# Performance work log

Hardware: AMD Instinct MI355X
Metric: run time of the kernel (lower is better)

Reference implementation:

```python
import jax, jax.numpy as jnp
import numpy as np

N_NODES = 50000
N_EDGES = 400000
D_IN, D_HID, D_LAT = 1024, 512, 256


def setup_inputs() -> dict:
    key = jax.random.key(0)
    k = jax.random.split(key, 6)
    x = jax.random.normal(k[0], (N_NODES, D_IN), dtype=jnp.float32)
    edge_index = jax.random.randint(k[1], (2, N_EDGES), 0, N_NODES, dtype=jnp.int32)
    # normalized adjacency weights (e.g., D^-1/2 A D^-1/2 values), positive
    edge_weight = jax.random.uniform(k[2], (N_EDGES,), dtype=jnp.float32)
    # Glorot-style init as in GCNConv.reset_parameters
    W1 = jax.random.normal(k[3], (D_IN, D_HID), dtype=jnp.float32) * (1.0 / np.sqrt(D_IN))
    b1 = jnp.zeros((D_HID,), dtype=jnp.float32)
    W2 = jax.random.normal(k[4], (D_HID, D_LAT), dtype=jnp.float32) * (1.0 / np.sqrt(D_HID))
    b2 = jnp.zeros((D_LAT,), dtype=jnp.float32)
    return {"x": x, "edge_index": edge_index, "edge_weight": edge_weight,
            "W1": W1, "b1": b1, "W2": W2, "b2": b2}


def _gcn_layer(h, src, dst, w, W, b):
    # GCNConv: spmm(adj, h @ W) + b
    s = h @ W                                   # [N, D_out] dense GEMM
    msg = s[src] * w[:, None]                   # [E, D_out] gather + scale
    agg = jax.ops.segment_sum(msg, dst, num_segments=N_NODES)  # scatter-add
    return agg + b


def reference(x, edge_index, edge_weight, W1, b1, W2, b2):
    # eval mode: F.dropout(training=False) is identity
    src, dst = edge_index[0], edge_index[1]
    h = jax.nn.relu(_gcn_layer(x, src, dst, edge_weight, W1, b1))
    out = jax.nn.relu(_gcn_layer(h, src, dst, edge_weight, W2, b2))
    return out
```

## Files before the change

kernel.cpp:

```cpp
#include <hip/hip_runtime.h>

typedef __attribute__((ext_vector_type(8))) short short8;
typedef __attribute__((ext_vector_type(4))) float floatx4;

#define GLOBAL_AS __attribute__((address_space(1)))
#define LDS_AS __attribute__((address_space(3)))

__device__ __forceinline__ void gload_lds16(const void* g, void* l) {
  __builtin_amdgcn_global_load_lds((const GLOBAL_AS unsigned int*)g,
                                   (LDS_AS unsigned int*)l, 16, 0, 0);
}

__device__ __forceinline__ unsigned short rnbf(float f) {
  unsigned int v = __builtin_bit_cast(unsigned int, f);
  return (unsigned short)((v + 0x7fff + ((v >> 16) & 1)) >> 16);
}
__device__ __forceinline__ float bflo(unsigned int u) {
  return __builtin_bit_cast(float, u << 16);
}
__device__ __forceinline__ float bfhi(unsigned int u) {
  return __builtin_bit_cast(float, u & 0xffff0000u);
}

#define TM 128
#define TN 128
#define BKE 64

__global__ __launch_bounds__(256) void gemm_bf16(
    const unsigned short* __restrict__ A,
    const unsigned short* __restrict__ Bt,
    unsigned short* __restrict__ C,
    int M, int N, int K) {
  __shared__ __align__(16) unsigned short As[TM * BKE];
  __shared__ __align__(16) unsigned short Bs[TN * BKE];

  const int tid  = threadIdx.x;
  const int wave = tid >> 6;
  const int lane = tid & 63;
  const int wm = wave >> 1, wn = wave & 1;
  const int l15 = lane & 15, quad = lane >> 4;

  const int bm = blockIdx.y * TM;
  const int bn = blockIdx.x * TN;

  floatx4 acc[4][4];
#pragma unroll
  for (int i = 0; i < 4; ++i)
#pragma unroll
    for (int j = 0; j < 4; ++j) acc[i][j] = (floatx4){0.f, 0.f, 0.f, 0.f};

  const unsigned short* aptr[4];
  const unsigned short* bptr[4];
  int ldsoff[4];
#pragma unroll
  for (int j = 0; j < 4; ++j) {
    int ci = (wave * 4 + j) * 64 + lane;
    int r  = ci >> 3;
    int cs = (ci & 7) ^ (r & 7);
    int arow = bm + r; if (arow >= M) arow = M - 1;
    aptr[j] = A  + (size_t)arow * K + cs * 8;
    bptr[j] = Bt + (size_t)(bn + r) * K + cs * 8;
    ldsoff[j] = (wave * 4 + j) * 64 * 8;
  }

  for (int k0 = 0; k0 < K; k0 += BKE) {
#pragma unroll
    for (int j = 0; j < 4; ++j) {
      gload_lds16(aptr[j] + k0, &As[ldsoff[j]]);
      gload_lds16(bptr[j] + k0, &Bs[ldsoff[j]]);
    }
    __syncthreads();
#pragma unroll
    for (int s = 0; s < 2; ++s) {
      short8 af[4], bf[4];
#pragma unroll
      for (int mt = 0; mt < 4; ++mt) {
        int mrow = wm * 64 + mt * 16 + l15;
        int sw = (s * 4 + quad) ^ (mrow & 7);
        af[mt] = *(const short8*)&As[(mrow * 8 + sw) * 8];
      }
#pragma unroll
      for (int nt = 0; nt < 4; ++nt) {
        int nrow = wn * 64 + nt * 16 + l15;
        int sw = (s * 4 + quad) ^ (nrow & 7);
        bf[nt] = *(const short8*)&Bs[(nrow * 8 + sw) * 8];
      }
#pragma unroll
      for (int mt = 0; mt < 4; ++mt)
#pragma unroll
        for (int nt = 0; nt < 4; ++nt)
          acc[mt][nt] = __builtin_amdgcn_mfma_f32_16x16x32_bf16(
              af[mt], bf[nt], acc[mt][nt], 0, 0, 0);
    }
    __syncthreads();
  }

#pragma unroll
  for (int mt = 0; mt < 4; ++mt) {
#pragma unroll
    for (int nt = 0; nt < 4; ++nt) {
      const int col = bn + wn * 64 + nt * 16 + l15;
#pragma unroll
      for (int i = 0; i < 4; ++i) {
        const int row = bm + wm * 64 + mt * 16 + quad * 4 + i;
        if (row < M) C[(size_t)row * N + col] = rnbf(acc[mt][nt][i]);
      }
    }
  }
}

__global__ __launch_bounds__(256) void cast_f32_to_bf16(
    const float* __restrict__ in, unsigned short* __restrict__ out,
    long long n4) {
  long long i = (long long)blockIdx.x * 256 + threadIdx.x;
  if (i >= n4) return;
  float4 v = ((const float4*)in)[i];
  ushort4 o;
  o.x = rnbf(v.x); o.y = rnbf(v.y); o.z = rnbf(v.z); o.w = rnbf(v.w);
  ((ushort4*)out)[i] = o;
}

__global__ __launch_bounds__(256) void transpose_cast_bf16(
    const float* __restrict__ in, unsigned short* __restrict__ out,
    int K, int N) {
  __shared__ float t[32][33];
  const int bx = blockIdx.x * 32;
  const int by = blockIdx.y * 32;
  const int tx = threadIdx.x & 31, ty = threadIdx.x >> 5;
#pragma unroll
  for (int j = 0; j < 4; ++j)
    t[ty + j * 8][tx] = in[(size_t)(by + ty + j * 8) * N + bx + tx];
  __syncthreads();
#pragma unroll
  for (int j = 0; j < 4; ++j)
    out[(size_t)(bx + ty + j * 8) * K + by + tx] = rnbf(t[tx][ty + j * 8]);
}

__global__ __launch_bounds__(256) void hist_dst(
    const int* __restrict__ dst, int* __restrict__ cnt, int E) {
  int e = blockIdx.x * blockDim.x + threadIdx.x;
  if (e < E) atomicAdd(&cnt[dst[e]], 1);
}

__global__ __launch_bounds__(1024) void scan_csr(
    int* __restrict__ cursor, int* __restrict__ rowptr, int n) {
  __shared__ int wsum[16];
  __shared__ int carry_s;
  const int t = threadIdx.x;
  const int wv = t >> 6, ln = t & 63;
  if (t == 0) carry_s = 0;
  __syncthreads();
  for (int base = 0; base < n; base += 1024) {
    const int i = base + t;
    const int v = (i < n) ? cursor[i] : 0;
    int x = v;
#pragma unroll
    for (int off = 1; off < 64; off <<= 1) {
      int y = __shfl_up(x, off, 64);
      if (ln >= off) x += y;
    }
    if (ln == 63) wsum[wv] = x;
    __syncthreads();
    if (t < 16) {
      int s = wsum[t];
#pragma unroll
      for (int off = 1; off < 16; off <<= 1) {
        int y = __shfl_up(s, off, 64);
        if (t >= off) s += y;
      }
      wsum[t] = s;
    }
    __syncthreads();
    const int prev  = (wv > 0) ? wsum[wv - 1] : 0;
    const int inc   = x + prev;
    const int carry = carry_s;
    if (i < n) {
      rowptr[i + 1] = carry + inc;
      cursor[i]     = carry + inc - v;
    }
    __syncthreads();
    if (t == 1023) carry_s = carry + inc;
  }
  if (t == 0) rowptr[0] = 0;
}

__global__ __launch_bounds__(256) void fill_csr(
    const int* __restrict__ dst, const int* __restrict__ src,
    const float* __restrict__ w, int* __restrict__ cursor,
    int* __restrict__ es, float* __restrict__ ws, int E) {
  int e = blockIdx.x * blockDim.x + threadIdx.x;
  if (e < E) {
    int pos = atomicAdd(&cursor[dst[e]], 1);
    es[pos] = src[e];
    ws[pos] = w[e];
  }
}

__global__ __launch_bounds__(256) void gather1_b2b(
    const unsigned short* __restrict__ S, const int* __restrict__ es,
    const float* __restrict__ ws, const int* __restrict__ rowptr,
    const float* __restrict__ bias, unsigned short* __restrict__ out, int Nn) {
  const int tn = threadIdx.x & 63;
  const int node = blockIdx.x * 4 + (threadIdx.x >> 6);
  if (node >= Nn) return;
  const int f = tn << 3;
  float acc[8] = {};
  const int beg = rowptr[node], end = rowptr[node + 1];
  for (int b = beg; b < end; b += 64) {
    const int m = end - b;
    int   sv_l = 0;
    float w_l  = 0.f;
    if (tn < m) { sv_l = es[b + tn]; w_l = ws[b + tn]; }
    const int cnt = (m < 64) ? m : 64;
    for (int i = 0; i < cnt; ++i) {
      const int   sv = __shfl(sv_l, i, 64);
      const float ww = __shfl(w_l, i, 64);
      const uint4 u = *(const uint4*)(S + (size_t)sv * 512 + f);
      acc[0] = fmaf(bflo(u.x), ww, acc[0]);
      acc[1] = fmaf(bfhi(u.x), ww, acc[1]);
      acc[2] = fmaf(bflo(u.y), ww, acc[2]);
      acc[3] = fmaf(bfhi(u.y), ww, acc[3]);
      acc[4] = fmaf(bflo(u.z), ww, acc[4]);
      acc[5] = fmaf(bfhi(u.z), ww, acc[5]);
      acc[6] = fmaf(bflo(u.w), ww, acc[6]);
      acc[7] = fmaf(bfhi(u.w), ww, acc[7]);
    }
  }
  float r[8];
#pragma unroll
  for (int j = 0; j < 8; ++j) r[j] = fmaxf(acc[j] + bias[f + j], 0.f);
  uint4 o;
  o.x = (unsigned int)rnbf(r[0]) | ((unsigned int)rnbf(r[1]) << 16);
  o.y = (unsigned int)rnbf(r[2]) | ((unsigned int)rnbf(r[3]) << 16);
  o.z = (unsigned int)rnbf(r[4]) | ((unsigned int)rnbf(r[5]) << 16);
  o.w = (unsigned int)rnbf(r[6]) | ((unsigned int)rnbf(r[7]) << 16);
  *(uint4*)(out + (size_t)node * 512 + f) = o;
}

__global__ __launch_bounds__(256) void gather2_b2f(
    const unsigned short* __restrict__ S, const int* __restrict__ es,
    const float* __restrict__ ws, const int* __restrict__ rowptr,
    const float* __restrict__ bias, float* __restrict__ out, int Nn) {
  const int tn = threadIdx.x & 31;
  const int node = blockIdx.x * 8 + (threadIdx.x >> 5);
  if (node >= Nn) return;
  const int f = tn << 3;
  float acc[8] = {};
  const int beg = rowptr[node], end = rowptr[node + 1];
  for (int b = beg; b < end; b += 32) {
    const int m = end - b;
    int   sv_l = 0;
    float w_l  = 0.f;
    if (tn < m) { sv_l = es[b + tn]; w_l = ws[b + tn]; }
    const int cnt = (m < 32) ? m : 32;
    for (int i = 0; i < cnt; ++i) {
      const int   sv = __shfl(sv_l, i, 32);
      const float ww = __shfl(w_l, i, 32);
      const uint4 u = *(const uint4*)(S + (size_t)sv * 256 + f);
      acc[0] = fmaf(bflo(u.x), ww, acc[0]);
      acc[1] = fmaf(bfhi(u.x), ww, acc[1]);
      acc[2] = fmaf(bflo(u.y), ww, acc[2]);
      acc[3] = fmaf(bfhi(u.y), ww, acc[3]);
      acc[4] = fmaf(bflo(u.z), ww, acc[4]);
      acc[5] = fmaf(bfhi(u.z), ww, acc[5]);
      acc[6] = fmaf(bflo(u.w), ww, acc[6]);
      acc[7] = fmaf(bfhi(u.w), ww, acc[7]);
    }
  }
  float4 o1, o2;
  o1.x = fmaxf(acc[0] + bias[f + 0], 0.f);
  o1.y = fmaxf(acc[1] + bias[f + 1], 0.f);
  o1.z = fmaxf(acc[2] + bias[f + 2], 0.f);
  o1.w = fmaxf(acc[3] + bias[f + 3], 0.f);
  o2.x = fmaxf(acc[4] + bias[f + 4], 0.f);
  o2.y = fmaxf(acc[5] + bias[f + 5], 0.f);
  o2.z = fmaxf(acc[6] + bias[f + 6], 0.f);
  o2.w = fmaxf(acc[7] + bias[f + 7], 0.f);
  *(float4*)(out + (size_t)node * 256 + f) = o1;
  *(float4*)(out + (size_t)node * 256 + f + 4) = o2;
}

extern "C" void kernel_launch(void* const* d_in, const int* in_sizes, int n_in,
                              void* d_out, int out_size, void* d_ws, size_t ws_size,
                              hipStream_t stream) {
  const float* x  = (const float*)d_in[0];
  const int*   ei = (const int*)d_in[1];
  const float* ew = (const float*)d_in[2];
  const float* W1 = (const float*)d_in[3];
  const float* b1 = (const float*)d_in[4];
  const float* W2 = (const float*)d_in[5];
  const float* b2 = (const float*)d_in[6];

  const int D_IN = 1024, D_HID = 512, D_LAT = 256;
  const int Nn = in_sizes[0] / D_IN;
  const int E  = in_sizes[2];
  const int* src  = ei;
  const int* dstp = ei + E;

  char* base = (char*)d_ws;
  const size_t szA = (size_t)Nn * D_IN * 2;
  const size_t szB = (size_t)Nn * D_HID * 2;
  unsigned short* xb  = (unsigned short*)base;
  unsigned short* hb  = (unsigned short*)base;
  unsigned short* s1  = (unsigned short*)(base + szA);
  unsigned short* s2  = (unsigned short*)(base + szA);
  char* tail = base + szA + szB;
  unsigned short* W1t = (unsigned short*)tail;
  unsigned short* W2t = W1t + (size_t)D_IN * D_HID;
  int*   rowptr = (int*)(W2t + (size_t)D_HID * D_LAT);
  int*   cursor = rowptr + (Nn + 1);
  int*   es     = cursor + Nn;
  float* wsrt   = (float*)(es + E);

  hipMemsetAsync(cursor, 0, (size_t)Nn * sizeof(int), stream);
  hist_dst<<<(E + 255) / 256, 256, 0, stream>>>(dstp, cursor, E);
  scan_csr<<<1, 1024, 0, stream>>>(cursor, rowptr, Nn);
  fill_csr<<<(E + 255) / 256, 256, 0, stream>>>(dstp, src, ew, cursor, es, wsrt, E);

  long long n4 = (long long)Nn * D_IN / 4;
  cast_f32_to_bf16<<<(int)((n4 + 255) / 256), 256, 0, stream>>>(x, xb, n4);
  transpose_cast_bf16<<<dim3(D_HID / 32, D_IN / 32), 256, 0, stream>>>(
      W1, W1t, D_IN, D_HID);
  transpose_cast_bf16<<<dim3(D_LAT / 32, D_HID / 32), 256, 0, stream>>>(
      W2, W2t, D_HID, D_LAT);

  dim3 g1(D_HID / TN, (Nn + TM - 1) / TM);
  gemm_bf16<<<g1, 256, 0, stream>>>(xb, W1t, s1, Nn, D_HID, D_IN);
  gather1_b2b<<<(Nn + 3) / 4, 256, 0, stream>>>(
      s1, es, wsrt, rowptr, b1, hb, Nn);

  dim3 g2(D_LAT / TN, (Nn + TM - 1) / TM);
  gemm_bf16<<<g2, 256, 0, stream>>>(hb, W2t, s2, Nn, D_LAT, D_HID);
  gather2_b2f<<<(Nn + 7) / 8, 256, 0, stream>>>(
      s2, es, wsrt, rowptr, b2, (float*)d_out, Nn);
}
```

Measured before the change: 605.2 us.

## Fuse preprocessing kernels, remap GEMM tiles per XCD, single-pass scan

Merges the x cast, destination histogram and both weight transpose-casts into one launch, with block ranges assigned to each task. The GEMM block index is remapped so consecutive tiles land on the same XCD, aiming for better L2 reuse of A and B rows. The CSR scan changes from a serial loop over 1024-element chunks with barriers to a per-thread segmented scan, trading coalescing for fewer synchronizations. Fusion removes launch overhead and lets independent preprocessing overlap, but hardcodes the weight dimensions and block counts.

```diff
diff --git a/kernel.cpp b/kernel.cpp
--- a/kernel.cpp
+++ b/kernel.cpp
@@ -40,8 +40,13 @@
   const int wm = wave >> 1, wn = wave & 1;
   const int l15 = lane & 15, quad = lane >> 4;
 
-  const int bm = blockIdx.y * TM;
-  const int bn = blockIdx.x * TN;
+  const int nwg = gridDim.x * gridDim.y;
+  const int bid = blockIdx.y * gridDim.x + blockIdx.x;
+  const int q = nwg >> 3, r = nwg & 7;
+  const int xcd = bid & 7, off = bid >> 3;
+  const int lid = ((xcd < r) ? xcd * (q + 1) : r * (q + 1) + (xcd - r) * q) + off;
+  const int bm = (lid / gridDim.x) * TM;
+  const int bn = (lid % gridDim.x) * TN;
 
   floatx4 acc[4][4];
 #pragma unroll
@@ -55,11 +60,11 @@
 #pragma unroll
   for (int j = 0; j < 4; ++j) {
     int ci = (wave * 4 + j) * 64 + lane;
-    int r  = ci >> 3;
-    int cs = (ci & 7) ^ (r & 7);
-    int arow = bm + r; if (arow >= M) arow = M - 1;
+    int rr = ci >> 3;
+    int cs = (ci & 7) ^ (rr & 7);
+    int arow = bm + rr; if (arow >= M) arow = M - 1;
     aptr[j] = A  + (size_t)arow * K + cs * 8;
-    bptr[j] = Bt + (size_t)(bn + r) * K + cs * 8;
+    bptr[j] = Bt + (size_t)(bn + rr) * K + cs * 8;
     ldsoff[j] = (wave * 4 + j) * 64 * 8;
   }
 
@@ -109,77 +114,93 @@
   }
 }
 
-__global__ __launch_bounds__(256) void cast_f32_to_bf16(
-    const float* __restrict__ in, unsigned short* __restrict__ out,
-    long long n4) {
-  long long i = (long long)blockIdx.x * 256 + threadIdx.x;
-  if (i >= n4) return;
-  float4 v = ((const float4*)in)[i];
-  ushort4 o;
-  o.x = rnbf(v.x); o.y = rnbf(v.y); o.z = rnbf(v.z); o.w = rnbf(v.w);
-  ((ushort4*)out)[i] = o;
-}
-
-__global__ __launch_bounds__(256) void transpose_cast_bf16(
-    const float* __restrict__ in, unsigned short* __restrict__ out,
-    int K, int N) {
-  __shared__ float t[32][33];
-  const int bx = blockIdx.x * 32;
-  const int by = blockIdx.y * 32;
-  const int tx = threadIdx.x & 31, ty = threadIdx.x >> 5;
-#pragma unroll
-  for (int j = 0; j < 4; ++j)
-    t[ty + j * 8][tx] = in[(size_t)(by + ty + j * 8) * N + bx + tx];
+#define PRE_CAST_B 1024
+#define PRE_HIST_B 512
+#define PRE_W1_B 512
+#define PRE_W2_B 128
+
+__global__ __launch_bounds__(256) void pre_fused(
+    const float* __restrict__ x, unsigned short* __restrict__ xb, long long n4,
+    const int* __restrict__ dst, int* __restrict__ cursor, int E,
+    const float* __restrict__ W1, unsigned short* __restrict__ W1t,
+    const float* __restrict__ W2, unsigned short* __restrict__ W2t) {
+  __shared__ float tile[32][33];
+  const int b = blockIdx.x, t = threadIdx.x;
+  if (b < PRE_CAST_B) {
+    for (long long i = (long long)b * 256 + t; i < n4;
+         i += (long long)PRE_CAST_B * 256) {
+      float4 v = ((const float4*)x)[i];
+      ushort4 o;
+      o.x = rnbf(v.x); o.y = rnbf(v.y); o.z = rnbf(v.z); o.w = rnbf(v.w);
+      ((ushort4*)xb)[i] = o;
+    }
+  } else if (b < PRE_CAST_B + PRE_HIST_B) {
+    const int bb = b - PRE_CAST_B;
+    for (int e = bb * 256 + t; e < E; e += PRE_HIST_B * 256)
+      atomicAdd(&cursor[dst[e]], 1);
+  } else if (b < PRE_CAST_B + PRE_HIST_B + PRE_W1_B) {
+    const int id = b - (PRE_CAST_B + PRE_HIST_B);
+    const int bx = (id & 15) * 32, by = (id >> 4) * 32;
+    const int tx = t & 31, ty = t >> 5;
+#pragma unroll
+    for (int j = 0; j < 4; ++j)
+      tile[ty + j * 8][tx] = W1[(size_t)(by + ty + j * 8) * 512 + bx + tx];
+    __syncthreads();
+#pragma unroll
+    for (int j = 0; j < 4; ++j)
+      W1t[(size_t)(bx + ty + j * 8) * 1024 + by + tx] = rnbf(tile[tx][ty + j * 8]);
+  } else {
+    const int id = b - (PRE_CAST_B + PRE_HIST_B + PRE_W1_B);
+    const int bx = (id & 7) * 32, by = (id >> 3) * 32;
+    const int tx = t & 31, ty = t >> 5;
+#pragma unroll
+    for (int j = 0; j < 4; ++j)
+      tile[ty + j * 8][tx] = W2[(size_t)(by + ty + j * 8) * 256 + bx + tx];
+    __syncthreads();
+#pragma unroll
+    for (int j = 0; j < 4; ++j)
+      W2t[(size_t)(bx + ty + j * 8) * 512 + by + tx] = rnbf(tile[tx][ty + j * 8]);
+  }
+}
+
+__global__ __launch_bounds__(1024) void scan_one(
+    int* cursor, int* __restrict__ rowptr, int n) {
+  __shared__ int wsum[16];
+  const int t = threadIdx.x, ln = t & 63, wv = t >> 6;
+  const int SEG = (n + 1023) >> 10;
+  const int beg = t * SEG;
+  int s = 0;
+  for (int k = 0; k < SEG; ++k) {
+    const int i = beg + k;
+    if (i < n) s += cursor[i];
+  }
+  int xinc = s;
+#pragma unroll
+  for (int o = 1; o < 64; o <<= 1) {
+    int y = __shfl_up(xinc, o, 64);
+    if (ln >= o) xinc += y;
+  }
+  if (ln == 63) wsum[wv] = xinc;
   __syncthreads();
-#pragma unroll
-  for (int j = 0; j < 4; ++j)
-    out[(size_t)(bx + ty + j * 8) * K + by + tx] = rnbf(t[tx][ty + j * 8]);
-}
-
-__global__ __launch_bounds__(256) void hist_dst(
-    const int* __restrict__ dst, int* __restrict__ cnt, int E) {
-  int e = blockIdx.x * blockDim.x + threadIdx.x;
-  if (e < E) atomicAdd(&cnt[dst[e]], 1);
-}
-
-__global__ __launch_bounds__(1024) void scan_csr(
-    int* __restrict__ cursor, int* __restrict__ rowptr, int n) {
-  __shared__ int wsum[16];
-  __shared__ int carry_s;
-  const int t = threadIdx.x;
-  const int wv = t >> 6, ln = t & 63;
-  if (t == 0) carry_s = 0;
+  if (t < 16) {
+    int v = wsum[t];
+#pragma unroll
+    for (int o = 1; o < 16; o <<= 1) {
+      int y = __shfl_up(v, o, 64);
+      if (t >= o) v += y;
+    }
+    wsum[t] = v;
+  }
   __syncthreads();
-  for (int base = 0; base < n; base += 1024) {
-    const int i = base + t;
-    const int v = (i < n) ? cursor[i] : 0;
-    int x = v;
-#pragma unroll
-    for (int off = 1; off < 64; off <<= 1) {
-      int y = __shfl_up(x, off, 64);
-      if (ln >= off) x += y;
-    }
-    if (ln == 63) wsum[wv] = x;
-    __syncthreads();
-    if (t < 16) {
-      int s = wsum[t];
-#pragma unroll
-      for (int off = 1; off < 16; off <<= 1) {
-        int y = __shfl_up(s, off, 64);
-        if (t >= off) s += y;
-      }
-      wsum[t] = s;
-    }
-    __syncthreads();
-    const int prev  = (wv > 0) ? wsum[wv - 1] : 0;
-    const int inc   = x + prev;
-    const int carry = carry_s;
+  int run = ((wv > 0) ? wsum[wv - 1] : 0) + xinc - s;
+  for (int k = 0; k < SEG; ++k) {
+    const int i = beg + k;
     if (i < n) {
-      rowptr[i + 1] = carry + inc;
-      cursor[i]     = carry + inc - v;
-    }
-    __syncthreads();
-    if (t == 1023) carry_s = carry + inc;
+      const int v = cursor[i];
+      cursor[i] = run;
+      rowptr[i + 1] = run + v;
+      run += v;
+    }
   }
   if (t == 0) rowptr[0] = 0;
 }
@@ -312,17 +333,13 @@
   int*   es     = cursor + Nn;
   float* wsrt   = (float*)(es + E);
 
+  long long n4 = (long long)Nn * D_IN / 4;
+
   hipMemsetAsync(cursor, 0, (size_t)Nn * sizeof(int), stream);
-  hist_dst<<<(E + 255) / 256, 256, 0, stream>>>(dstp, cursor, E);
-  scan_csr<<<1, 1024, 0, stream>>>(cursor, rowptr, Nn);
+  pre_fused<<<PRE_CAST_B + PRE_HIST_B + PRE_W1_B + PRE_W2_B, 256, 0, stream>>>(
+      x, xb, n4, dstp, cursor, E, W1, W1t, W2, W2t);
+  scan_one<<<1, 1024, 0, stream>>>(cursor, rowptr, Nn);
   fill_csr<<<(E + 255) / 256, 256, 0, stream>>>(dstp, src, ew, cursor, es, wsrt, E);
-
-  long long n4 = (long long)Nn * D_IN / 4;
-  cast_f32_to_bf16<<<(int)((n4 + 255) / 256), 256, 0, stream>>>(x, xb, n4);
-  transpose_cast_bf16<<<dim3(D_HID / 32, D_IN / 32), 256, 0, stream>>>(
-      W1, W1t, D_IN, D_HID);
-  transpose_cast_bf16<<<dim3(D_LAT / 32, D_HID / 32), 256, 0, stream>>>(
-      W2, W2t, D_HID, D_LAT);
 
   dim3 g1(D_HID / TN, (Nn + TM - 1) / TM);
   gemm_bf16<<<g1, 256, 0, stream>>>(xb, W1t, s1, Nn, D_HID, D_IN);
```

New measurement: 686.2 us. 13.4% more time.
